# Performance work log

Hardware: AMD Instinct MI355X
Metric: run time of the kernel (lower is better)

The kernel has to match this reference:

```python
import jax, jax.numpy as jnp
import numpy as np

B, I, O = 262144, 128, 128


def setup_inputs() -> dict:
    key = jax.random.key(0)
    k1, k2, k3, k4 = jax.random.split(key, 4)
    # coordinate-like inputs in [-1, 1]
    x = jax.random.uniform(k1, (B, I), dtype=jnp.float32, minval=-1.0, maxval=1.0)
    # complex weight w = s * exp(i*theta): |w| = s (close to 1 so |w|^x stays stable),
    # angle(w) = theta, matching the torch init where complex_weight = cos(a) + i sin(a).
    theta = jax.random.uniform(k2, (O, I), dtype=jnp.float32, minval=-np.pi, maxval=np.pi)
    scale = jnp.exp(0.1 * jax.random.normal(k3, (O, I), dtype=jnp.float32))
    w_real = scale * jnp.cos(theta)
    w_imag = scale * jnp.sin(theta)
    bias = jax.random.uniform(k4, (O,), dtype=jnp.float32, minval=-np.pi, maxval=np.pi)
    return {"x": x, "w_real": w_real, "w_imag": w_imag, "bias": bias}


def reference(x, w_real, w_imag, bias):
    # complex_weight.abs() and .angle() from real/imag components
    abs_w = jnp.sqrt(w_real * w_real + w_imag * w_imag)      # [O, I]
    angle_w = jnp.arctan2(w_imag, w_real)                     # [O, I]
    # magnitude = prod_i |w|_{o,i} ** x_{b,i}  ==  exp(x @ log|w|^T)
    # (algebraic rewrite of the O(B*O*I) pow+prod into a GEMM + pointwise exp)
    magnitude = jnp.exp(jnp.einsum('bi,oi->bo', x, jnp.log(abs_w)))  # [B, O]
    # y = F.linear(x, angle, bias)
    y = jnp.einsum('bi,oi->bo', x, angle_w) + bias            # [B, O]
    return jnp.cos(y) * magnitude
```

## Files before the change

kernel.cpp:

```cpp
#include <hip/hip_runtime.h>


typedef __attribute__((ext_vector_type(8))) short bf16x8;
typedef __attribute__((ext_vector_type(4))) float f32x4;

#define MFMA(a, b, c) __builtin_amdgcn_mfma_f32_16x16x32_bf16((a), (b), (c), 0, 0, 0)

__device__ __forceinline__ void block_sync_lds() {
    __builtin_amdgcn_sched_barrier(0);
    asm volatile("s_waitcnt lgkmcnt(0)" ::: "memory");
    __builtin_amdgcn_s_barrier();
    __builtin_amdgcn_sched_barrier(0);
}

__device__ __forceinline__ unsigned short f2bf_rne(float f) {
    unsigned u = __float_as_uint(f);
    unsigned r = u + 0x7FFFu + ((u >> 16) & 1u);
    return (unsigned short)(r >> 16);
}

__device__ __forceinline__ void bf16_split(float f, unsigned short& hi, unsigned short& lo) {
    unsigned uh = __float_as_uint(f) & 0xFFFF0000u;
    hi = (unsigned short)(uh >> 16);
    lo = f2bf_rne(f - __uint_as_float(uh));
}

__device__ __forceinline__ void cvt_pair(float f0, float f1, unsigned& h, unsigned& l) {
    unsigned u0 = __float_as_uint(f0), u1 = __float_as_uint(f1);
    unsigned uh0 = u0 & 0xFFFF0000u, uh1 = u1 & 0xFFFF0000u;
    h = (uh0 >> 16) | uh1;
    float r0 = f0 - __uint_as_float(uh0);
    float r1 = f1 - __uint_as_float(uh1);
    unsigned v0 = __float_as_uint(r0), v1 = __float_as_uint(r1);
    v0 = v0 + 0x7FFFu + ((v0 >> 16) & 1u);
    v1 = v1 + 0x7FFFu + ((v1 >> 16) & 1u);
    l = (v0 >> 16) | (v1 & 0xFFFF0000u);
}

__global__ void ces_prep(const float* __restrict__ wr, const float* __restrict__ wi,
                         unsigned short* __restrict__ wsplit) {
    int idx = blockIdx.x * 256 + threadIdx.x;
    float a = wr[idx], b = wi[idx];
    float r2 = a * a + b * b;
    float ang = atan2f(b, a);
    float lg = 0.5f * logf(r2);
    unsigned short ah, al, gh, gl;
    bf16_split(ang, ah, al);
    bf16_split(lg, gh, gl);
    wsplit[idx]         = ah;
    wsplit[16384 + idx] = al;
    wsplit[32768 + idx] = gh;
    wsplit[49152 + idx] = gl;
}

#define NT 16

__global__ __launch_bounds__(256, 2) void ces_main(
        const float* __restrict__ x,
        const unsigned short* __restrict__ wsplit,
        const float* __restrict__ bias,
        float* __restrict__ out) {
    __shared__ __align__(16) unsigned short smem[8192];
    char* smemb = (char*)smem;

    const int tid  = threadIdx.x;
    const int wave = tid >> 6;
    const int lane = tid & 63;
    const int quad = lane >> 4;
    const int l16  = lane & 15;
    const int n0   = wave * 32;

    bf16x8 wa_h[2][4], wa_l[2][4], wg_h[2][4], wg_l[2][4];
#pragma unroll
    for (int nt = 0; nt < 2; ++nt) {
        const int o = n0 + nt * 16 + l16;
#pragma unroll
        for (int ks = 0; ks < 4; ++ks) {
            const int off = o * 128 + ks * 32 + quad * 8;
            wa_h[nt][ks] = *(const bf16x8*)(wsplit + off);
            wa_l[nt][ks] = *(const bf16x8*)(wsplit + 16384 + off);
            wg_h[nt][ks] = *(const bf16x8*)(wsplit + 32768 + off);
            wg_l[nt][ks] = *(const bf16x8*)(wsplit + 49152 + off);
        }
    }
    float bias_v[2];
    bias_v[0] = bias[n0 + l16];
    bias_v[1] = bias[n0 + 16 + l16];

    const int srow = tid >> 4;
    const int schk = tid & 15;
    const int wb = (srow * 256 + schk * 16) ^ ((srow & 7) << 4);

    int rb[4];
#pragma unroll
    for (int ks = 0; ks < 4; ++ks)
        rb[ks] = (l16 * 256 + ks * 64 + quad * 16) ^ ((l16 & 7) << 4);

    const float* xb = x + (size_t)blockIdx.x * (NT * 2048) + srow * 128 + schk * 8;

    {
        float4 v0 = *(const float4*)(xb);
        float4 v1 = *(const float4*)(xb + 4);
        unsigned h0, l0, h1, l1, h2, l2, h3, l3;
        cvt_pair(v0.x, v0.y, h0, l0);
        cvt_pair(v0.z, v0.w, h1, l1);
        cvt_pair(v1.x, v1.y, h2, l2);
        cvt_pair(v1.z, v1.w, h3, l3);
        *(uint4*)(smemb + wb)        = make_uint4(h0, h1, h2, h3);
        *(uint4*)(smemb + wb + 4096) = make_uint4(l0, l1, l2, l3);
    }
    float4 pf0 = *(const float4*)(xb + 2048);
    float4 pf1 = *(const float4*)(xb + 2048 + 4);
    block_sync_lds();

    for (int i = 0; i < NT; ++i) {
        const int bo = (i & 1) << 13;

        f32x4 accY[2], accG[2];
        accY[0] = (f32x4){0.f, 0.f, 0.f, 0.f};
        accY[1] = (f32x4){0.f, 0.f, 0.f, 0.f};
        accG[0] = (f32x4){0.f, 0.f, 0.f, 0.f};
        accG[1] = (f32x4){0.f, 0.f, 0.f, 0.f};
#pragma unroll
        for (int ks = 0; ks < 4; ++ks) {
            bf16x8 a_h = *(const bf16x8*)(smemb + (bo + rb[ks]));
            bf16x8 a_l = *(const bf16x8*)(smemb + (bo + rb[ks] + 4096));
            accY[0] = MFMA(a_h, wa_h[0][ks], accY[0]);
            accG[0] = MFMA(a_h, wg_h[0][ks], accG[0]);
            accY[1] = MFMA(a_h, wa_h[1][ks], accY[1]);
            accG[1] = MFMA(a_h, wg_h[1][ks], accG[1]);
            accY[0] = MFMA(a_h, wa_l[0][ks], accY[0]);
            accG[0] = MFMA(a_h, wg_l[0][ks], accG[0]);
            accY[1] = MFMA(a_h, wa_l[1][ks], accY[1]);
            accG[1] = MFMA(a_h, wg_l[1][ks], accG[1]);
            accY[0] = MFMA(a_l, wa_h[0][ks], accY[0]);
            accG[0] = MFMA(a_l, wg_h[0][ks], accG[0]);
            accY[1] = MFMA(a_l, wa_h[1][ks], accY[1]);
            accG[1] = MFMA(a_l, wg_h[1][ks], accG[1]);
        }

        if (i + 1 < NT) {
            const int nbo = bo ^ 8192;
            unsigned h0, l0, h1, l1, h2, l2, h3, l3;
            cvt_pair(pf0.x, pf0.y, h0, l0);
            cvt_pair(pf0.z, pf0.w, h1, l1);
            cvt_pair(pf1.x, pf1.y, h2, l2);
            cvt_pair(pf1.z, pf1.w, h3, l3);
            *(uint4*)(smemb + (nbo + wb))        = make_uint4(h0, h1, h2, h3);
            *(uint4*)(smemb + (nbo + wb + 4096)) = make_uint4(l0, l1, l2, l3);
        }
        {
            int tn = i + 2;
            if (tn > NT - 1) tn = NT - 1;
            pf0 = *(const float4*)(xb + tn * 2048);
            pf1 = *(const float4*)(xb + tn * 2048 + 4);
        }

        block_sync_lds();

        {
            const size_t R0 = (size_t)(blockIdx.x * NT + i) * 16;
#pragma unroll
            for (int nt = 0; nt < 2; ++nt) {
                const int o = n0 + nt * 16 + l16;
#pragma unroll
                for (int r = 0; r < 4; ++r) {
                    float y = accY[nt][r] + bias_v[nt];
                    out[(R0 + quad * 4 + r) * 128 + o] = __cosf(y) * __expf(accG[nt][r]);
                }
            }
        }
    }
}

extern "C" void kernel_launch(void* const* d_in, const int* in_sizes, int n_in,
                              void* d_out, int out_size, void* d_ws, size_t ws_size,
                              hipStream_t stream) {
    const float* x    = (const float*)d_in[0];
    const float* wr   = (const float*)d_in[1];
    const float* wi   = (const float*)d_in[2];
    const float* bias = (const float*)d_in[3];
    float* out = (float*)d_out;
    unsigned short* wsplit = (unsigned short*)d_ws;

    ces_prep<<<64, 256, 0, stream>>>(wr, wi, wsplit);

    ces_main<<<1024, 256, 0, stream>>>(x, wsplit, bias, out);
}
```

Baseline: 254.9 us.

## Software-pipeline epilogue of previous tile into next tile's MFMA loop

Restructures the main loop into a templated tile body with ping-pong accumulators so that the cos/exp epilogue and global stores of tile i-1 are interleaved with the MFMA k-steps of tile i. The LDS staging (convert, store) and the global prefetch are also spread across specific k-steps. The goal is to hide transcendental and store latency behind matrix-core work. In exchange it doubles the accumulator registers, which could pressure the 2-waves-per-SIMD occupancy target.

```diff
diff --git a/kernel.cpp b/kernel.cpp
--- a/kernel.cpp
+++ b/kernel.cpp
@@ -55,6 +55,66 @@
 
 #define NT 16
 
+template<bool STAGE, bool EPI>
+__device__ __forceinline__ void tile_body(
+        char* smemb, const int bo_read, const int bo_write,
+        const int (&rb)[4], const int wb,
+        f32x4 (&cY)[2], f32x4 (&cG)[2],
+        f32x4 (&pY)[2], f32x4 (&pG)[2],
+        float4& pf0, float4& pf1, const float* pfsrc,
+        const bf16x8 (&wa_h)[2][4], const bf16x8 (&wa_l)[2][4],
+        const bf16x8 (&wg_h)[2][4], const bf16x8 (&wg_l)[2][4],
+        const float (&bias_v)[2], float* outp) {
+    cY[0] = (f32x4){0.f, 0.f, 0.f, 0.f};
+    cY[1] = (f32x4){0.f, 0.f, 0.f, 0.f};
+    cG[0] = (f32x4){0.f, 0.f, 0.f, 0.f};
+    cG[1] = (f32x4){0.f, 0.f, 0.f, 0.f};
+
+    unsigned sh[4], sl[4];
+
+#pragma unroll
+    for (int ks = 0; ks < 4; ++ks) {
+        bf16x8 a_h = *(const bf16x8*)(smemb + (bo_read + rb[ks]));
+        bf16x8 a_l = *(const bf16x8*)(smemb + (bo_read + rb[ks] + 4096));
+        cY[0] = MFMA(a_h, wa_h[0][ks], cY[0]);
+        cG[0] = MFMA(a_h, wg_h[0][ks], cG[0]);
+        cY[1] = MFMA(a_h, wa_h[1][ks], cY[1]);
+        cG[1] = MFMA(a_h, wg_h[1][ks], cG[1]);
+        cY[0] = MFMA(a_h, wa_l[0][ks], cY[0]);
+        cG[0] = MFMA(a_h, wg_l[0][ks], cG[0]);
+        cY[1] = MFMA(a_h, wa_l[1][ks], cY[1]);
+        cG[1] = MFMA(a_h, wg_l[1][ks], cG[1]);
+        cY[0] = MFMA(a_l, wa_h[0][ks], cY[0]);
+        cG[0] = MFMA(a_l, wg_h[0][ks], cG[0]);
+        cY[1] = MFMA(a_l, wa_h[1][ks], cY[1]);
+        cG[1] = MFMA(a_l, wg_h[1][ks], cG[1]);
+
+        if (EPI) {
+            const int nt = ks >> 1;
+            const int r0 = (ks & 1) * 2;
+#pragma unroll
+            for (int r = r0; r < r0 + 2; ++r) {
+                float y = pY[nt][r] + bias_v[nt];
+                outp[(size_t)r * 128 + nt * 16] = __cosf(y) * __expf(pG[nt][r]);
+            }
+        }
+        if (STAGE) {
+            if (ks == 0) {
+                cvt_pair(pf0.x, pf0.y, sh[0], sl[0]);
+                cvt_pair(pf0.z, pf0.w, sh[1], sl[1]);
+                cvt_pair(pf1.x, pf1.y, sh[2], sl[2]);
+                cvt_pair(pf1.z, pf1.w, sh[3], sl[3]);
+            } else if (ks == 1) {
+                *(uint4*)(smemb + (bo_write + wb))        = make_uint4(sh[0], sh[1], sh[2], sh[3]);
+                *(uint4*)(smemb + (bo_write + wb + 4096)) = make_uint4(sl[0], sl[1], sl[2], sl[3]);
+            } else if (ks == 2) {
+                pf0 = *(const float4*)(pfsrc);
+                pf1 = *(const float4*)(pfsrc + 4);
+            }
+        }
+    }
+}
+
 __global__ __launch_bounds__(256, 2) void ces_main(
         const float* __restrict__ x,
         const unsigned short* __restrict__ wsplit,
@@ -97,6 +157,10 @@
         rb[ks] = (l16 * 256 + ks * 64 + quad * 16) ^ ((l16 & 7) << 4);
 
     const float* xb = x + (size_t)blockIdx.x * (NT * 2048) + srow * 128 + schk * 8;
+    const size_t base = (size_t)blockIdx.x * NT;
+    float* outb = out + (size_t)quad * 4 * 128 + n0 + l16;
+
+    f32x4 aY[2], aG[2], bY[2], bG[2];
 
     {
         float4 v0 = *(const float4*)(xb);
@@ -113,61 +177,44 @@
     float4 pf1 = *(const float4*)(xb + 2048 + 4);
     block_sync_lds();
 
-    for (int i = 0; i < NT; ++i) {
-        const int bo = (i & 1) << 13;
-
-        f32x4 accY[2], accG[2];
-        accY[0] = (f32x4){0.f, 0.f, 0.f, 0.f};
-        accY[1] = (f32x4){0.f, 0.f, 0.f, 0.f};
-        accG[0] = (f32x4){0.f, 0.f, 0.f, 0.f};
-        accG[1] = (f32x4){0.f, 0.f, 0.f, 0.f};
-#pragma unroll
-        for (int ks = 0; ks < 4; ++ks) {
-            bf16x8 a_h = *(const bf16x8*)(smemb + (bo + rb[ks]));
-            bf16x8 a_l = *(const bf16x8*)(smemb + (bo + rb[ks] + 4096));
-            accY[0] = MFMA(a_h, wa_h[0][ks], accY[0]);
-            accG[0] = MFMA(a_h, wg_h[0][ks], accG[0]);
-            accY[1] = MFMA(a_h, wa_h[1][ks], accY[1]);
-            accG[1] = MFMA(a_h, wg_h[1][ks], accG[1]);
-            accY[0] = MFMA(a_h, wa_l[0][ks], accY[0]);
-            accG[0] = MFMA(a_h, wg_l[0][ks], accG[0]);
-            accY[1] = MFMA(a_h, wa_l[1][ks], accY[1]);
-            accG[1] = MFMA(a_h, wg_l[1][ks], accG[1]);
-            accY[0] = MFMA(a_l, wa_h[0][ks], accY[0]);
-            accG[0] = MFMA(a_l, wg_h[0][ks], accG[0]);
-            accY[1] = MFMA(a_l, wa_h[1][ks], accY[1]);
-            accG[1] = MFMA(a_l, wg_h[1][ks], accG[1]);
-        }
-
-        if (i + 1 < NT) {
-            const int nbo = bo ^ 8192;
-            unsigned h0, l0, h1, l1, h2, l2, h3, l3;
-            cvt_pair(pf0.x, pf0.y, h0, l0);
-            cvt_pair(pf0.z, pf0.w, h1, l1);
-            cvt_pair(pf1.x, pf1.y, h2, l2);
-            cvt_pair(pf1.z, pf1.w, h3, l3);
-            *(uint4*)(smemb + (nbo + wb))        = make_uint4(h0, h1, h2, h3);
-            *(uint4*)(smemb + (nbo + wb + 4096)) = make_uint4(l0, l1, l2, l3);
-        }
+    tile_body<true, false>(smemb, 0, 8192, rb, wb, aY, aG, bY, bG,
+                           pf0, pf1, xb + 2 * 2048,
+                           wa_h, wa_l, wg_h, wg_l, bias_v, outb);
+    block_sync_lds();
+
+    for (int i = 1; i + 1 < NT; i += 2) {
         {
-            int tn = i + 2;
-            if (tn > NT - 1) tn = NT - 1;
-            pf0 = *(const float4*)(xb + tn * 2048);
-            pf1 = *(const float4*)(xb + tn * 2048 + 4);
-        }
-
+            int tn = i + 2; if (tn > NT - 1) tn = NT - 1;
+            float* outp = outb + (base + i - 1) * (16 * 128);
+            tile_body<true, true>(smemb, 8192, 0, rb, wb, bY, bG, aY, aG,
+                                  pf0, pf1, xb + tn * 2048,
+                                  wa_h, wa_l, wg_h, wg_l, bias_v, outp);
+        }
         block_sync_lds();
-
         {
-            const size_t R0 = (size_t)(blockIdx.x * NT + i) * 16;
-#pragma unroll
-            for (int nt = 0; nt < 2; ++nt) {
-                const int o = n0 + nt * 16 + l16;
-#pragma unroll
-                for (int r = 0; r < 4; ++r) {
-                    float y = accY[nt][r] + bias_v[nt];
-                    out[(R0 + quad * 4 + r) * 128 + o] = __cosf(y) * __expf(accG[nt][r]);
-                }
+            int tn = i + 3; if (tn > NT - 1) tn = NT - 1;
+            float* outp = outb + (base + i) * (16 * 128);
+            tile_body<true, true>(smemb, 0, 8192, rb, wb, aY, aG, bY, bG,
+                                  pf0, pf1, xb + tn * 2048,
+                                  wa_h, wa_l, wg_h, wg_l, bias_v, outp);
+        }
+        block_sync_lds();
+    }
+
+    {
+        float* outp = outb + (base + NT - 2) * (16 * 128);
+        tile_body<false, true>(smemb, 8192, 0, rb, wb, bY, bG, aY, aG,
+                               pf0, pf1, xb,
+                               wa_h, wa_l, wg_h, wg_l, bias_v, outp);
+    }
+    {
+        float* outp = outb + (base + NT - 1) * (16 * 128);
+#pragma unroll
+        for (int nt = 0; nt < 2; ++nt) {
+#pragma unroll
+            for (int r = 0; r < 4; ++r) {
+                float y = bY[nt][r] + bias_v[nt];
+                outp[(size_t)r * 128 + nt * 16] = __cosf(y) * __expf(bG[nt][r]);
             }
         }
     }
```

Result: no change. 257.1 us (+0.9%).
